# Kernel tuning notes

Measured on AMD Instinct MI355X. Metric: run time of the kernel, lower is better.

Reference implementation:

```python
import jax, jax.numpy as jnp
import numpy as np

C = 1024
KSIZE = 7
PAD = 3
STRIDE = 1


def _dwconv(x, w):
    # x: [B, C, L], w: [C, 1, K] depthwise (feature_group_count=C)
    return jax.lax.conv_general_dilated(
        x, w,
        window_strides=(STRIDE,),
        padding=[(PAD, PAD)],
        feature_group_count=C,
        dimension_numbers=('NCH', 'OIH', 'NCH'),
    )


def setup_inputs() -> dict:
    key = jax.random.key(0)
    kx, kq, kk, kv = jax.random.split(key, 4)
    B, L = 8, 4096
    x = jax.random.normal(kx, (B, C, L), dtype=jnp.float32)
    # depthwise conv weights, fan_in = 1*K per group -> kaiming-ish scale
    scale = 1.0 / np.sqrt(KSIZE)
    q_w = jax.random.normal(kq, (C, 1, KSIZE), dtype=jnp.float32) * scale
    k_w = jax.random.normal(kk, (C, 1, KSIZE), dtype=jnp.float32) * scale
    v_w = jax.random.normal(kv, (C, 1, KSIZE), dtype=jnp.float32) * scale
    return {"x": x, "q_w": q_w, "k_w": k_w, "v_w": v_w}


def reference(x, q_w, k_w, v_w):
    sqrt_dk = np.sqrt(C).astype(np.float32)
    q = _dwconv(x, q_w)  # [B, C, L']
    k = _dwconv(x, k_w)
    v = _dwconv(x, v_w)
    score = jnp.einsum('bcl,bdl->bcd', q, k) / sqrt_dk  # [B, C, C]
    attn = jax.nn.softmax(score, axis=-1)
    out = jnp.einsum('bcd,bdl->bcl', attn, v)  # [B, C, L']
    return out
```

## Files before the change

kernel.cpp:

```cpp
#include <hip/hip_runtime.h>
#include <hip/hip_bf16.h>

typedef unsigned short u16;
typedef unsigned int u32;
typedef __attribute__((ext_vector_type(8))) __bf16 bf16x8;
typedef __attribute__((ext_vector_type(4))) float f32x4;
typedef __attribute__((ext_vector_type(4))) unsigned int u32x4;

#define CC 1024
#define LL 4096
#define NB 8

#define VMCNT(n) asm volatile("s_waitcnt vmcnt(" #n ")" ::: "memory")
#define LGKMC(n) asm volatile("s_waitcnt lgkmcnt(" #n ")" ::: "memory")
#define BAR()    asm volatile("s_barrier" ::: "memory")

__device__ __forceinline__ u16 f2bf(float f) {
  union { float f; unsigned u; } v; v.f = f;
  unsigned u = v.u;
  return (u16)((u + 0x7fffu + ((u >> 16) & 1u)) >> 16);
}

__device__ __forceinline__ u16 bfc(float f) {
  __bf16 h = (__bf16)f;
  return __builtin_bit_cast(u16, h);
}

__device__ __forceinline__ float bf2f(u32 u) {
  return __builtin_bit_cast(float, u << 16);
}

__device__ __forceinline__ void gload_lds16(const void* g, void* l) {
  __builtin_amdgcn_global_load_lds(
      (const __attribute__((address_space(1))) void*)g,
      (__attribute__((address_space(3))) void*)l, 16, 0, 0);
}

__global__ __launch_bounds__(256) void dwconv_qkv(
    const float* __restrict__ x, const float* __restrict__ qw,
    const float* __restrict__ kw, const float* __restrict__ vw,
    u16* __restrict__ qo, u16* __restrict__ ko, u16* __restrict__ vto)
{
  __shared__ u16 vs[64][68];
  const int t  = threadIdx.x;
  const int l0 = blockIdx.x << 6;
  const int c0 = blockIdx.y << 6;
  const int b  = blockIdx.z;
  const int cc = t >> 2;
  const int g  = t & 3;
  const int c  = c0 + cc;
  const float* xr = x + ((size_t)(b * CC + c)) * LL;
  const int li0 = g << 4;
  const int p0  = l0 + li0;

  float xv[24];
  if (l0 != 0 && l0 != LL - 64) {
    const float4* base = (const float4*)(xr + p0 - 4);
#pragma unroll
    for (int j = 0; j < 6; ++j) {
      float4 f = base[j];
      xv[4 * j + 0] = f.x; xv[4 * j + 1] = f.y;
      xv[4 * j + 2] = f.z; xv[4 * j + 3] = f.w;
    }
  } else {
#pragma unroll
    for (int i = 0; i < 24; ++i) {
      int gl = p0 - 4 + i;
      xv[i] = ((unsigned)gl < (unsigned)LL) ? xr[gl] : 0.f;
    }
  }

  float wq[7], wk[7], wv[7];
#pragma unroll
  for (int j = 0; j < 7; ++j) {
    wq[j] = qw[c * 7 + j]; wk[j] = kw[c * 7 + j]; wv[j] = vw[c * 7 + j];
  }

  const int wgrp = cc >> 4;
  alignas(16) u16 qv[16], kv[16];
#pragma unroll
  for (int li = 0; li < 16; ++li) {
    float aq = 0.f, ak = 0.f, av = 0.f;
#pragma unroll
    for (int j = 0; j < 7; ++j) {
      float xf = xv[li + 1 + j];
      aq = fmaf(xf, wq[j], aq);
      ak = fmaf(xf, wk[j], ak);
      av = fmaf(xf, wv[j], av);
    }
    qv[li] = bfc(aq);
    kv[li] = bfc(ak);
    vs[li0 + li][(cc & 15) + ((wgrp ^ g) << 4)] = bfc(av);
  }
  size_t qoff = ((size_t)(b * CC + c)) * LL + p0;
  ((u32x4*)(qo + qoff))[0] = ((const u32x4*)qv)[0];
  ((u32x4*)(ko + qoff))[0] = ((const u32x4*)kv)[0];
  ((u32x4*)(qo + qoff))[1] = ((const u32x4*)qv)[1];
  ((u32x4*)(ko + qoff))[1] = ((const u32x4*)kv)[1];

  LGKMC(0);
  BAR();
  const int q4 = t & 3;
  const int ll = t >> 2;
  const int sb = q4 ^ (ll >> 4);
  bf16x8 v0 = *(const bf16x8*)&vs[ll][sb << 4];
  bf16x8 v1 = *(const bf16x8*)&vs[ll][(sb << 4) + 8];
  size_t voff = ((size_t)(b * LL) + l0 + ll) * CC + c0 + (q4 << 4);
  *(bf16x8*)(vto + voff)     = v0;
  *(bf16x8*)(vto + voff + 8) = v1;
}

__global__ __launch_bounds__(512, 2) void gemm256p(
    const u16* __restrict__ A, int lda, size_t sA,
    const u16* __restrict__ B, int ldb, size_t sB,
    void* __restrict__ C0, void* __restrict__ C1, int ldc, size_t sC,
    int K, int ksplit, int mapmode, int obf16)
{
  __shared__ alignas(16) u16 lds[65536];
  const int t    = threadIdx.x;
  const int lane = t & 63, wave = t >> 6;
  const int wrow = wave >> 2, wcol = wave & 3;
  int bx, by, z;
  if (mapmode == 0) {
    int wg = blockIdx.x; z = wg & 15; int r = wg >> 4; bx = r & 3; by = r >> 2;
  } else {
    int wg = blockIdx.x; z = wg & 7; by = (wg >> 3) & 3; bx = wg >> 5;
  }
  const int bm = by << 8, bn = bx << 8;
  const int batch = (ksplit == 2) ? (z >> 1) : z;
  const int split = (ksplit == 2) ? (z & 1) : 0;
  const int Ks    = (ksplit == 2) ? (K >> 1) : K;
  const u16* Ab = A + (size_t)batch * sA + (size_t)split * Ks;
  const u16* Bb = B + (size_t)batch * sB + (size_t)split * Ks;

  const int srow = lane >> 3;
  const int scol = ((lane & 7) ^ srow) << 3;
  const u16* pA[2][2]; const u16* pB[2][2];
  int dstOff[2];
#pragma unroll
  for (int i = 0; i < 2; ++i) {
    int cch = wave * 2 + i;
    dstOff[i] = cch * 1024 + lane * 16;
    pA[0][i] = Ab + (size_t)(bm + cch * 8 + srow) * lda + scol;
    pA[1][i] = pA[0][i] + (size_t)128 * lda;
    pB[0][i] = Bb + (size_t)(bn + cch * 8 + srow) * ldb + scol;
    pB[1][i] = pB[0][i] + (size_t)128 * ldb;
  }

#define STGH(P, h, base, koff)                                            \
  do {                                                                    \
    gload_lds16(P[h][0] + (koff), (char*)lds + (base) + dstOff[0]);       \
    gload_lds16(P[h][1] + (koff), (char*)lds + (base) + dstOff[1]);       \
  } while (0)

  const int r15 = lane & 15, kq = lane >> 4, swz = r15 & 7;
  int rowA[8], rowB[4], colK[2];
#pragma unroll
  for (int m = 0; m < 8; ++m) rowA[m] = (wrow * 128 + m * 16 + r15) * 128;
#pragma unroll
  for (int n = 0; n < 4; ++n) rowB[n] = 32768 + (wcol * 64 + n * 16 + r15) * 128;
#pragma unroll
  for (int s = 0; s < 2; ++s) colK[s] = (((s * 4 + kq) ^ swz)) << 4;

  f32x4 acc[8][4];
#pragma unroll
  for (int i = 0; i < 8; ++i)
#pragma unroll
    for (int j = 0; j < 4; ++j) acc[i][j] = f32x4{0.f, 0.f, 0.f, 0.f};

  const int NT = Ks >> 6;

  STGH(pA, 0, 0, 0);            STGH(pA, 1, 16384, 0);
  STGH(pB, 0, 32768, 0);        STGH(pB, 1, 49152, 0);
  STGH(pA, 0, 65536 + 0, 64);   STGH(pA, 1, 65536 + 16384, 64);
  STGH(pB, 0, 65536 + 32768, 64);
  VMCNT(6);
  BAR();

  const char* L = (const char*)lds;
  for (int tt = 0; tt < NT; ++tt) {
    const int d = tt & 1;
    const int dbase = d << 16, sbase = (d ^ 1) << 16;
    const int kN1 = (tt + 1) << 6, kN2 = (tt + 2) << 6;
    bf16x8 a0[4], aK1a[4], b0[4];
#pragma unroll
    for (int m = 0; m < 4; ++m) a0[m] = *(const bf16x8*)(L + dbase + rowA[m] + colK[0]);
#pragma unroll
    for (int n = 0; n < 4; ++n) b0[n] = *(const bf16x8*)(L + dbase + rowB[n] + colK[0]);
    if (tt + 1 < NT) STGH(pB, 1, sbase + 49152, kN1);
#pragma unroll
    for (int m = 0; m < 4; ++m) aK1a[m] = *(const bf16x8*)(L + dbase + rowA[m] + colK[1]);
    LGKMC(4);
    __builtin_amdgcn_sched_barrier(0);
    __builtin_amdgcn_s_setprio(1);
#pragma unroll
    for (int m = 0; m < 4; ++m)
#pragma unroll
      for (int n = 0; n < 4; ++n)
        acc[m][n] = __builtin_amdgcn_mfma_f32_16x16x32_bf16(a0[m], b0[n], acc[m][n], 0, 0, 0);
    __builtin_amdgcn_s_setprio(0);
    bf16x8 a4[4], aK1b[4];
#pragma unroll
    for (int m = 0; m < 4; ++m) a4[m] = *(const bf16x8*)(L + dbase + rowA[m + 4] + colK[0]);
#pragma unroll
    for (int m = 0; m < 4; ++m) aK1b[m] = *(const bf16x8*)(L + dbase + rowA[m + 4] + colK[1]);
    LGKMC(4);
    __builtin_amdgcn_sched_barrier(0);
    __builtin_amdgcn_s_setprio(1);
#pragma unroll
    for (int m = 0; m < 4; ++m)
#pragma unroll
      for (int n = 0; n < 4; ++n)
        acc[m + 4][n] = __builtin_amdgcn_mfma_f32_16x16x32_bf16(a4[m], b0[n], acc[m + 4][n], 0, 0, 0);
    __builtin_amdgcn_s_setprio(0);
    BAR();
    bf16x8 b1[4];
#pragma unroll
    for (int n = 0; n < 4; ++n) b1[n] = *(const bf16x8*)(L + dbase + rowB[n] + colK[1]);
    if (tt + 2 < NT) STGH(pA, 0, dbase + 0, kN2);
    LGKMC(0);
    __builtin_amdgcn_sched_barrier(0);
    __builtin_amdgcn_s_setprio(1);
#pragma unroll
    for (int m = 0; m < 4; ++m)
#pragma unroll
      for (int n = 0; n < 4; ++n)
        acc[m][n] = __builtin_amdgcn_mfma_f32_16x16x32_bf16(aK1a[m], b1[n], acc[m][n], 0, 0, 0);
    __builtin_amdgcn_s_setprio(0);
    BAR();
    if (tt + 2 < NT) { STGH(pA, 1, dbase + 16384, kN2); STGH(pB, 0, dbase + 32768, kN2); }
    __builtin_amdgcn_s_setprio(1);
#pragma unroll
    for (int m = 0; m < 4; ++m)
#pragma unroll
      for (int n = 0; n < 4; ++n)
        acc[m + 4][n] = __builtin_amdgcn_mfma_f32_16x16x32_bf16(aK1b[m], b1[n], acc[m + 4][n], 0, 0, 0);
    __builtin_amdgcn_s_setprio(0);
    if (tt < NT - 2) { VMCNT(6); } else { VMCNT(0); }
    BAR();
  }
#undef STGH

  const int row0 = bm + wrow * 128 + kq * 4;
  const int col0 = bn + wcol * 64 + r15;
  if (obf16) {
    u16* Cb = (u16*)(split ? C1 : C0) + (size_t)batch * sC;
#pragma unroll
    for (int m = 0; m < 8; ++m)
#pragma unroll
      for (int n = 0; n < 4; ++n) {
        const int r   = row0 + m * 16;
        const int col = col0 + n * 16;
#pragma unroll
        for (int rr = 0; rr < 4; ++rr)
          Cb[(size_t)(r + rr) * ldc + col] = bfc(acc[m][n][rr]);
      }
  } else {
    float* Cb = (float*)(split ? C1 : C0) + (size_t)batch * sC;
#pragma unroll
    for (int m = 0; m < 8; ++m)
#pragma unroll
      for (int n = 0; n < 4; ++n) {
        const int r   = row0 + m * 16;
        const int col = col0 + n * 16;
#pragma unroll
        for (int rr = 0; rr < 4; ++rr)
          Cb[(size_t)(r + rr) * ldc + col] = acc[m][n][rr];
      }
  }
}

__global__ __launch_bounds__(256) void softmax_rows(
    u16* __restrict__ score, const u16* __restrict__ part)
{
  __shared__ float rmax[4], rsum[4];
  const int t = threadIdx.x;
  const int lane = t & 63, wv = t >> 6;
  u16* sp = score + ((size_t)blockIdx.x << 10);
  const u16* pp = part + ((size_t)blockIdx.x << 10);
  uint2 va = *(const uint2*)(sp + (t << 2));
  uint2 vb = *(const uint2*)(pp + (t << 2));
  const float scale = 0.03125f;
  float a0 = (bf2f(va.x & 0xffffu) + bf2f(vb.x & 0xffffu)) * scale;
  float a1 = (bf2f(va.x >> 16)     + bf2f(vb.x >> 16))     * scale;
  float a2 = (bf2f(va.y & 0xffffu) + bf2f(vb.y & 0xffffu)) * scale;
  float a3 = (bf2f(va.y >> 16)     + bf2f(vb.y >> 16))     * scale;
  float m = fmaxf(fmaxf(a0, a1), fmaxf(a2, a3));
#pragma unroll
  for (int o = 1; o < 64; o <<= 1) m = fmaxf(m, __shfl_xor(m, o, 64));
  if (lane == 0) rmax[wv] = m;
  __syncthreads();
  m = fmaxf(fmaxf(rmax[0], rmax[1]), fmaxf(rmax[2], rmax[3]));
  float e0 = __expf(a0 - m), e1 = __expf(a1 - m);
  float e2 = __expf(a2 - m), e3 = __expf(a3 - m);
  float s = e0 + e1 + e2 + e3;
#pragma unroll
  for (int o = 1; o < 64; o <<= 1) s += __shfl_xor(s, o, 64);
  if (lane == 0) rsum[wv] = s;
  __syncthreads();
  s = rsum[0] + rsum[1] + rsum[2] + rsum[3];
  const float inv = 1.0f / s;
  uint2 ob;
  ob.x = (u32)f2bf(e0 * inv) | ((u32)f2bf(e1 * inv) << 16);
  ob.y = (u32)f2bf(e2 * inv) | ((u32)f2bf(e3 * inv) << 16);
  *(uint2*)(sp + (t << 2)) = ob;
}

extern "C" void kernel_launch(void* const* d_in, const int* in_sizes, int n_in,
                              void* d_out, int out_size, void* d_ws, size_t ws_size,
                              hipStream_t stream) {
  const float* x  = (const float*)d_in[0];
  const float* qw = (const float*)d_in[1];
  const float* kw = (const float*)d_in[2];
  const float* vw = (const float*)d_in[3];
  float* out = (float*)d_out;
  char* ws = (char*)d_ws;

  u16*  q     = (u16*)ws;
  u16*  k     = (u16*)(ws + 67108864);
  u16*  vt    = (u16*)(ws + 134217728);
  u16*  score = (u16*)(ws + 201326592);
  u16*  part  = (u16*)d_out;

  dim3 cg(LL / 64, CC / 64, NB);
  dwconv_qkv<<<cg, 256, 0, stream>>>(x, qw, kw, vw, q, k, vt);

  gemm256p<<<dim3(256), 512, 0, stream>>>(q, LL, (size_t)CC * LL,
                                          k, LL, (size_t)CC * LL,
                                          (void*)score, (void*)part,
                                          CC, (size_t)CC * CC,
                                          LL, 2, 0, 1);

  softmax_rows<<<NB * CC, 256, 0, stream>>>(score, part);

  gemm256p<<<dim3(512), 512, 0, stream>>>(score, CC, (size_t)CC * CC,
                                          vt, CC, (size_t)LL * CC,
                                          (void*)out, nullptr,
                                          LL, (size_t)CC * LL,
                                          CC, 1, 1, 0);
}
```

Measured before the change: 241.4 us.

## Split QK^T GEMM four ways along K and double dwconv tile width

The score GEMM now uses a 4-way split over the L dimension instead of 2-way, which doubles its grid to 512 workgroups for better CU occupancy. It writes four bf16 partial score buffers that softmax sums. The dwconv kernel now processes 128 positions per block in two 64-wide halves with separate LDS buffers, halving the grid and amortizing weight loads. This adds extra partial-buffer traffic and bf16 rounding of more partials, and it uses additional workspace and output memory as scratch.

```diff
diff --git a/kernel.cpp b/kernel.cpp
--- a/kernel.cpp
+++ b/kernel.cpp
@@ -41,9 +41,9 @@
     const float* __restrict__ kw, const float* __restrict__ vw,
     u16* __restrict__ qo, u16* __restrict__ ko, u16* __restrict__ vto)
 {
-  __shared__ u16 vs[64][68];
+  __shared__ u16 vs[2][64][68];
   const int t  = threadIdx.x;
-  const int l0 = blockIdx.x << 6;
+  const int l0 = blockIdx.x << 7;
   const int c0 = blockIdx.y << 6;
   const int b  = blockIdx.z;
   const int cc = t >> 2;
@@ -51,22 +51,36 @@
   const int c  = c0 + cc;
   const float* xr = x + ((size_t)(b * CC + c)) * LL;
   const int li0 = g << 4;
-  const int p0  = l0 + li0;
-
-  float xv[24];
-  if (l0 != 0 && l0 != LL - 64) {
-    const float4* base = (const float4*)(xr + p0 - 4);
+  const int pA  = l0 + li0;
+  const int pB  = pA + 64;
+
+  float xvA[24], xvB[24];
+  if (l0 != 0) {
+    const float4* base = (const float4*)(xr + pA - 4);
 #pragma unroll
     for (int j = 0; j < 6; ++j) {
       float4 f = base[j];
-      xv[4 * j + 0] = f.x; xv[4 * j + 1] = f.y;
-      xv[4 * j + 2] = f.z; xv[4 * j + 3] = f.w;
+      xvA[4*j] = f.x; xvA[4*j+1] = f.y; xvA[4*j+2] = f.z; xvA[4*j+3] = f.w;
     }
   } else {
 #pragma unroll
     for (int i = 0; i < 24; ++i) {
-      int gl = p0 - 4 + i;
-      xv[i] = ((unsigned)gl < (unsigned)LL) ? xr[gl] : 0.f;
+      int gl = pA - 4 + i;
+      xvA[i] = ((unsigned)gl < (unsigned)LL) ? xr[gl] : 0.f;
+    }
+  }
+  if (l0 != LL - 128) {
+    const float4* base = (const float4*)(xr + pB - 4);
+#pragma unroll
+    for (int j = 0; j < 6; ++j) {
+      float4 f = base[j];
+      xvB[4*j] = f.x; xvB[4*j+1] = f.y; xvB[4*j+2] = f.z; xvB[4*j+3] = f.w;
+    }
+  } else {
+#pragma unroll
+    for (int i = 0; i < 24; ++i) {
+      int gl = pB - 4 + i;
+      xvB[i] = ((unsigned)gl < (unsigned)LL) ? xr[gl] : 0.f;
     }
   }
 
@@ -77,59 +91,94 @@
   }
 
   const int wgrp = cc >> 4;
-  alignas(16) u16 qv[16], kv[16];
-#pragma unroll
-  for (int li = 0; li < 16; ++li) {
-    float aq = 0.f, ak = 0.f, av = 0.f;
-#pragma unroll
-    for (int j = 0; j < 7; ++j) {
-      float xf = xv[li + 1 + j];
-      aq = fmaf(xf, wq[j], aq);
-      ak = fmaf(xf, wk[j], ak);
-      av = fmaf(xf, wv[j], av);
-    }
-    qv[li] = bfc(aq);
-    kv[li] = bfc(ak);
-    vs[li0 + li][(cc & 15) + ((wgrp ^ g) << 4)] = bfc(av);
-  }
-  size_t qoff = ((size_t)(b * CC + c)) * LL + p0;
-  ((u32x4*)(qo + qoff))[0] = ((const u32x4*)qv)[0];
-  ((u32x4*)(ko + qoff))[0] = ((const u32x4*)kv)[0];
-  ((u32x4*)(qo + qoff))[1] = ((const u32x4*)qv)[1];
-  ((u32x4*)(ko + qoff))[1] = ((const u32x4*)kv)[1];
-
+  const int vcol = (cc & 15) + ((wgrp ^ g) << 4);
+  const size_t qoffA = ((size_t)(b * CC + c)) * LL + pA;
+
+  {
+    alignas(16) u16 qv[16], kv[16];
+#pragma unroll
+    for (int li = 0; li < 16; ++li) {
+      float aq = 0.f, ak = 0.f, av = 0.f;
+#pragma unroll
+      for (int j = 0; j < 7; ++j) {
+        float xf = xvA[li + 1 + j];
+        aq = fmaf(xf, wq[j], aq);
+        ak = fmaf(xf, wk[j], ak);
+        av = fmaf(xf, wv[j], av);
+      }
+      qv[li] = bfc(aq); kv[li] = bfc(ak);
+      vs[0][li0 + li][vcol] = bfc(av);
+    }
+    ((u32x4*)(qo + qoffA))[0] = ((const u32x4*)qv)[0];
+    ((u32x4*)(ko + qoffA))[0] = ((const u32x4*)kv)[0];
+    ((u32x4*)(qo + qoffA))[1] = ((const u32x4*)qv)[1];
+    ((u32x4*)(ko + qoffA))[1] = ((const u32x4*)kv)[1];
+  }
   LGKMC(0);
   BAR();
+
   const int q4 = t & 3;
   const int ll = t >> 2;
   const int sb = q4 ^ (ll >> 4);
-  bf16x8 v0 = *(const bf16x8*)&vs[ll][sb << 4];
-  bf16x8 v1 = *(const bf16x8*)&vs[ll][(sb << 4) + 8];
-  size_t voff = ((size_t)(b * LL) + l0 + ll) * CC + c0 + (q4 << 4);
-  *(bf16x8*)(vto + voff)     = v0;
-  *(bf16x8*)(vto + voff + 8) = v1;
+  {
+    bf16x8 v0 = *(const bf16x8*)&vs[0][ll][sb << 4];
+    bf16x8 v1 = *(const bf16x8*)&vs[0][ll][(sb << 4) + 8];
+    size_t voff = ((size_t)(b * LL) + l0 + ll) * CC + c0 + (q4 << 4);
+    *(bf16x8*)(vto + voff)     = v0;
+    *(bf16x8*)(vto + voff + 8) = v1;
+  }
+  {
+    alignas(16) u16 qv[16], kv[16];
+#pragma unroll
+    for (int li = 0; li < 16; ++li) {
+      float aq = 0.f, ak = 0.f, av = 0.f;
+#pragma unroll
+      for (int j = 0; j < 7; ++j) {
+        float xf = xvB[li + 1 + j];
+        aq = fmaf(xf, wq[j], aq);
+        ak = fmaf(xf, wk[j], ak);
+        av = fmaf(xf, wv[j], av);
+      }
+      qv[li] = bfc(aq); kv[li] = bfc(ak);
+      vs[1][li0 + li][vcol] = bfc(av);
+    }
+    ((u32x4*)(qo + qoffA + 64))[0] = ((const u32x4*)qv)[0];
+    ((u32x4*)(ko + qoffA + 64))[0] = ((const u32x4*)kv)[0];
+    ((u32x4*)(qo + qoffA + 64))[1] = ((const u32x4*)qv)[1];
+    ((u32x4*)(ko + qoffA + 64))[1] = ((const u32x4*)kv)[1];
+  }
+  LGKMC(0);
+  BAR();
+  {
+    bf16x8 v0 = *(const bf16x8*)&vs[1][ll][sb << 4];
+    bf16x8 v1 = *(const bf16x8*)&vs[1][ll][(sb << 4) + 8];
+    size_t voff = ((size_t)(b * LL) + l0 + 64 + ll) * CC + c0 + (q4 << 4);
+    *(bf16x8*)(vto + voff)     = v0;
+    *(bf16x8*)(vto + voff + 8) = v1;
+  }
 }
 
 __global__ __launch_bounds__(512, 2) void gemm256p(
     const u16* __restrict__ A, int lda, size_t sA,
     const u16* __restrict__ B, int ldb, size_t sB,
-    void* __restrict__ C0, void* __restrict__ C1, int ldc, size_t sC,
-    int K, int ksplit, int mapmode, int obf16)
+    void* __restrict__ C0, void* __restrict__ C1,
+    void* __restrict__ C2, void* __restrict__ C3, int ldc, size_t sC,
+    int K, int mapmode, int obf16)
 {
   __shared__ alignas(16) u16 lds[65536];
   const int t    = threadIdx.x;
   const int lane = t & 63, wave = t >> 6;
   const int wrow = wave >> 2, wcol = wave & 3;
-  int bx, by, z;
+  int bx, by, batch, split, Ks;
   if (mapmode == 0) {
-    int wg = blockIdx.x; z = wg & 15; int r = wg >> 4; bx = r & 3; by = r >> 2;
+    int wg = blockIdx.x; int z = wg & 31; int r = wg >> 5;
+    bx = r & 3; by = r >> 2;
+    batch = z >> 2; split = z & 3; Ks = K >> 2;
   } else {
-    int wg = blockIdx.x; z = wg & 7; by = (wg >> 3) & 3; bx = wg >> 5;
+    int wg = blockIdx.x; int z = wg & 7; by = (wg >> 3) & 3; bx = wg >> 5;
+    batch = z; split = 0; Ks = K;
   }
   const int bm = by << 8, bn = bx << 8;
-  const int batch = (ksplit == 2) ? (z >> 1) : z;
-  const int split = (ksplit == 2) ? (z & 1) : 0;
-  const int Ks    = (ksplit == 2) ? (K >> 1) : K;
   const u16* Ab = A + (size_t)batch * sA + (size_t)split * Ks;
   const u16* Bb = B + (size_t)batch * sB + (size_t)split * Ks;
 
@@ -241,10 +290,11 @@
   }
 #undef STGH
 
+  void* Cv = (split & 2) ? ((split & 1) ? C3 : C2) : ((split & 1) ? C1 : C0);
   const int row0 = bm + wrow * 128 + kq * 4;
   const int col0 = bn + wcol * 64 + r15;
   if (obf16) {
-    u16* Cb = (u16*)(split ? C1 : C0) + (size_t)batch * sC;
+    u16* Cb = (u16*)Cv + (size_t)batch * sC;
 #pragma unroll
     for (int m = 0; m < 8; ++m)
 #pragma unroll
@@ -256,7 +306,7 @@
           Cb[(size_t)(r + rr) * ldc + col] = bfc(acc[m][n][rr]);
       }
   } else {
-    float* Cb = (float*)(split ? C1 : C0) + (size_t)batch * sC;
+    float* Cb = (float*)Cv + (size_t)batch * sC;
 #pragma unroll
     for (int m = 0; m < 8; ++m)
 #pragma unroll
@@ -271,20 +321,26 @@
 }
 
 __global__ __launch_bounds__(256) void softmax_rows(
-    u16* __restrict__ score, const u16* __restrict__ part)
+    u16* __restrict__ score, const u16* __restrict__ p1,
+    const u16* __restrict__ p2, const u16* __restrict__ p3)
 {
   __shared__ float rmax[4], rsum[4];
   const int t = threadIdx.x;
   const int lane = t & 63, wv = t >> 6;
   u16* sp = score + ((size_t)blockIdx.x << 10);
-  const u16* pp = part + ((size_t)blockIdx.x << 10);
-  uint2 va = *(const uint2*)(sp + (t << 2));
-  uint2 vb = *(const uint2*)(pp + (t << 2));
+  uint2 v0 = *(const uint2*)(sp + (t << 2));
+  uint2 v1 = *(const uint2*)(p1 + ((size_t)blockIdx.x << 10) + (t << 2));
+  uint2 v2 = *(const uint2*)(p2 + ((size_t)blockIdx.x << 10) + (t << 2));
+  uint2 v3 = *(const uint2*)(p3 + ((size_t)blockIdx.x << 10) + (t << 2));
   const float scale = 0.03125f;
-  float a0 = (bf2f(va.x & 0xffffu) + bf2f(vb.x & 0xffffu)) * scale;
-  float a1 = (bf2f(va.x >> 16)     + bf2f(vb.x >> 16))     * scale;
-  float a2 = (bf2f(va.y & 0xffffu) + bf2f(vb.y & 0xffffu)) * scale;
-  float a3 = (bf2f(va.y >> 16)     + bf2f(vb.y >> 16))     * scale;
+  float a0 = (bf2f(v0.x & 0xffffu) + bf2f(v1.x & 0xffffu) +
+              bf2f(v2.x & 0xffffu) + bf2f(v3.x & 0xffffu)) * scale;
+  float a1 = (bf2f(v0.x >> 16) + bf2f(v1.x >> 16) +
+              bf2f(v2.x >> 16) + bf2f(v3.x >> 16)) * scale;
+  float a2 = (bf2f(v0.y & 0xffffu) + bf2f(v1.y & 0xffffu) +
+              bf2f(v2.y & 0xffffu) + bf2f(v3.y & 0xffffu)) * scale;
+  float a3 = (bf2f(v0.y >> 16) + bf2f(v1.y >> 16) +
+              bf2f(v2.y >> 16) + bf2f(v3.y >> 16)) * scale;
   float m = fmaxf(fmaxf(a0, a1), fmaxf(a2, a3));
 #pragma unroll
   for (int o = 1; o < 64; o <<= 1) m = fmaxf(m, __shfl_xor(m, o, 64));
@@ -320,22 +376,25 @@
   u16*  k     = (u16*)(ws + 67108864);
   u16*  vt    = (u16*)(ws + 134217728);
   u16*  score = (u16*)(ws + 201326592);
-  u16*  part  = (u16*)d_out;
-
-  dim3 cg(LL / 64, CC / 64, NB);
+  u16*  p1    = (u16*)(ws + 218103808);
+  u16*  p2    = (u16*)d_out;
+  u16*  p3    = (u16*)d_out + 8388608;
+
+  dim3 cg(LL / 128, CC / 64, NB);
   dwconv_qkv<<<cg, 256, 0, stream>>>(x, qw, kw, vw, q, k, vt);
 
-  gemm256p<<<dim3(256), 512, 0, stream>>>(q, LL, (size_t)CC * LL,
+  gemm256p<<<dim3(512), 512, 0, stream>>>(q, LL, (size_t)CC * LL,
                                           k, LL, (size_t)CC * LL,
-                                          (void*)score, (void*)part,
+                                          (void*)score, (void*)p1,
+                                          (void*)p2, (void*)p3,
                                           CC, (size_t)CC * CC,
-                                          LL, 2, 0, 1);
-
-  softmax_rows<<<NB * CC, 256, 0, stream>>>(score, part);
+                                          LL, 0, 1);
+
+  softmax_rows<<<NB * CC, 256, 0, stream>>>(score, p1, p2, p3);
 
   gemm256p<<<dim3(512), 512, 0, stream>>>(score, CC, (size_t)CC * CC,
                                           vt, CC, (size_t)LL * CC,
-                                          (void*)out, nullptr,
+                                          (void*)out, nullptr, nullptr, nullptr,
                                           LL, (size_t)CC * LL,
-                                          CC, 1, 1, 0);
-}
+                                          CC, 1, 0);
+}
```

Result: slower. 257.9 us (+6.8%).
